# Performance work log

Hardware: AMD Instinct MI355X
Metric: run time of the kernel (lower is better)

## Reference

```python
import jax, jax.numpy as jnp
import numpy as np

B, F_IN, T = 128, 64, 512       # batch, input_features, seq_len
H, L = 512, 3                   # hidden_dim, num_layers
F_OUT, W_OUT = 8, 64            # output_features, output_window


def setup_inputs() -> dict:
    key = jax.random.key(0)
    ks = jax.random.split(key, 13)
    s = 1.0 / np.sqrt(H)  # torch nn.LSTM init scale
    f32 = jnp.float32
    return {
        "x": jax.random.normal(ks[0], (B, F_IN, T), f32),
        # encoder LSTM params (gate order i,f,g,o like torch)
        "enc_Wih0": jax.random.normal(ks[1], (4 * H, F_IN), f32) * s,
        "enc_Wih": jax.random.normal(ks[2], (L - 1, 4 * H, H), f32) * s,
        "enc_Whh": jax.random.normal(ks[3], (L, 4 * H, H), f32) * s,
        "enc_bih": jax.random.normal(ks[4], (L, 4 * H), f32) * s,
        "enc_bhh": jax.random.normal(ks[5], (L, 4 * H), f32) * s,
        # decoder LSTM params
        "dec_Wih0": jax.random.normal(ks[6], (4 * H, F_OUT), f32) * s,
        "dec_Wih": jax.random.normal(ks[7], (L - 1, 4 * H, H), f32) * s,
        "dec_Whh": jax.random.normal(ks[8], (L, 4 * H, H), f32) * s,
        "dec_bih": jax.random.normal(ks[9], (L, 4 * H), f32) * s,
        "dec_bhh": jax.random.normal(ks[10], (L, 4 * H), f32) * s,
        # output projection
        "fc_w": jax.random.normal(ks[11], (F_OUT, H), f32) * s,
        "fc_b": jax.random.normal(ks[12], (F_OUT,), f32) * s,
    }


def _cell(inp, h, c, Wi, Wh, bi, bh):
    # torch LSTM cell: gates = W_ih x + b_ih + W_hh h + b_hh, order i,f,g,o
    g = inp @ Wi.T + h @ Wh.T + bi + bh
    i, f, gg, o = jnp.split(g, 4, axis=-1)
    c_new = jax.nn.sigmoid(f) * c + jax.nn.sigmoid(i) * jnp.tanh(gg)
    h_new = jax.nn.sigmoid(o) * jnp.tanh(c_new)
    return h_new, c_new


def _stack_step(x_t, h, c, Wih0, Wih, Whh, bih, bhh):
    # one time step through all L layers; h,c: [L,B,H]
    inp = x_t
    hs, cs = [], []
    for l in range(Whh.shape[0]):
        Wi = Wih0 if l == 0 else Wih[l - 1]
        h_new, c_new = _cell(inp, h[l], c[l], Wi, Whh[l], bih[l], bhh[l])
        hs.append(h_new)
        cs.append(c_new)
        inp = h_new
    return jnp.stack(hs), jnp.stack(cs), inp


def reference(x, enc_Wih0, enc_Wih, enc_Whh, enc_bih, enc_bhh,
              dec_Wih0, dec_Wih, dec_Whh, dec_bih, dec_bhh, fc_w, fc_b):
    b = x.shape[0]
    # ---- encoder: x.permute(0,2,1) -> [B,T,F_IN], scan over time ----
    x_seq = jnp.transpose(x, (2, 0, 1))  # [T,B,F_IN]
    h0 = jnp.zeros((L, b, H), x.dtype)
    c0 = jnp.zeros((L, b, H), x.dtype)

    def enc_step(carry, x_t):
        h, c = carry
        h, c, _ = _stack_step(x_t, h, c, enc_Wih0, enc_Wih, enc_Whh, enc_bih, enc_bhh)
        return (h, c), None

    (h, c), _ = jax.lax.scan(enc_step, (h0, c0), x_seq)

    # ---- last_x = x[:, -1, :][:, 0:F_OUT] (target_coin_index=0) ----
    dec_in = x[:, -1, :F_OUT]  # [B, F_OUT]

    def dec_step(carry, _):
        h, c, inp = carry
        h, c, top = _stack_step(inp, h, c, dec_Wih0, dec_Wih, dec_Whh, dec_bih, dec_bhh)
        pred = top @ fc_w.T + fc_b  # [B, F_OUT]
        return (h, c, pred), pred

    _, preds = jax.lax.scan(dec_step, (h, c, dec_in), None, length=W_OUT)  # [W,B,F_OUT]
    # torch returns cat over time [B,W,F_OUT] then permute(0,2,1) -> [B,F_OUT,W]
    return jnp.transpose(preds, (1, 2, 0))
```

## Files before the change

kernel.cpp:

```cpp
#include <hip/hip_runtime.h>
#include <hip/hip_cooperative_groups.h>

namespace cg = cooperative_groups;

#define B_    128
#define H_    512
#define T_    512
#define FIN_  64
#define FOUT_ 8
#define WOUT_ 64
#define G4H_  2048

#define NBLK  192
#define NTHR  512
#define RD    4

typedef __attribute__((ext_vector_type(8))) _Float16 half8;
typedef __attribute__((ext_vector_type(4))) float f32x4;
typedef unsigned short u16;
typedef unsigned int u32;

#define LOSCALE   4096.0f
#define LOINV     0.000244140625f

struct Params {
  const float *x, *eWih0, *eWih, *eWhh, *ebih, *ebhh;
  const float *dWih0, *dWih, *dWhh, *dbih, *dbhh, *fcw, *fcb;
  float *out; float *ws;
};

__device__ __forceinline__ float sigm(float x) { return 1.0f / (1.0f + __expf(-x)); }
__device__ __forceinline__ float tanhf_(float x) {
  float e = __expf(-2.0f * fabsf(x));
  return copysignf((1.0f - e) / (1.0f + e), x);
}
__device__ __forceinline__ u16 h2u(_Float16 h) {
  union { _Float16 f; u16 u; } v; v.f = h; return v.u;
}
__device__ __forceinline__ void split16(float w, u16& hi, u16& lo) {
  _Float16 h = (_Float16)w;
  _Float16 l = (_Float16)((w - (float)h) * LOSCALE);
  hi = h2u(h); lo = h2u(l);
}

__device__ __forceinline__ int aload(const int* p) {
  return __hip_atomic_load(p, __ATOMIC_RELAXED, __HIP_MEMORY_SCOPE_AGENT);
}
__device__ __forceinline__ void wait_all(const int* a, const int* b, const int* c) {
  if (threadIdx.x == 0) {
    while (a && aload(a) < 64) __builtin_amdgcn_s_sleep(1);
    while (b && aload(b) < 64) __builtin_amdgcn_s_sleep(1);
    while (c && aload(c) < 64) __builtin_amdgcn_s_sleep(1);
    __threadfence();
  }
  __syncthreads();
}
__device__ __forceinline__ void signal_f(int* f) {
  __syncthreads();
  if (threadIdx.x == 0) {
    __threadfence();
    __hip_atomic_fetch_add(f, 1, __ATOMIC_RELAXED, __HIP_MEMORY_SCOPE_AGENT);
  }
}

__device__ void stage_w(u16* WbHi, u16* WbLo, const float* Wi, int Kreal, int K0pad,
                        const float* Wh, int j0) {
  const int rowlen = K0pad + H_;
  for (int n = 0; n < 32; ++n) {
    const int gr = (n >> 3) * H_ + j0 + (n & 7);
    const float* s0 = Wi + (size_t)gr * Kreal;
    const float* s1 = Wh + (size_t)gr * H_;
    const int sw = (n & 7) << 3;
    for (int k = threadIdx.x; k < rowlen; k += NTHR) {
      float w = (k < K0pad) ? ((k < Kreal) ? s0[k] : 0.0f) : s1[k - K0pad];
      u16 hi, lo; split16(w, hi, lo);
      int kk = k ^ sw;
      WbHi[n * 1024 + kk] = hi;
      WbLo[n * 1024 + kk] = lo;
    }
  }
}

template <int NC0, bool DEC0, bool FC>
__device__ __forceinline__ void cell(
    const u16* __restrict__ WbHi, const u16* __restrict__ WbLo,
    float* __restrict__ gl, float* __restrict__ predl,
    const float* __restrict__ bias_s, const float* __restrict__ fcw_s,
    const u16* __restrict__ i0h, const u16* __restrict__ i0l, const int ld0,
    const float* __restrict__ pr_in,
    const u16* __restrict__ iHh, const u16* __restrict__ iHl,
    u16* __restrict__ ohh, u16* __restrict__ ohl, const int j0,
    float* __restrict__ creg, float* __restrict__ pr_out) {
  const int tid = threadIdx.x;
  const int lane = tid & 63, lr = lane & 15, lg = lane >> 4;
  const int m0 = (tid >> 6) << 4;
  const int mb = m0 + lr;
  const int sw = (lr & 7) << 3;

  f32x4 acc0 = {0.f, 0.f, 0.f, 0.f}, acc1 = {0.f, 0.f, 0.f, 0.f};
  f32x4 acc0L = {0.f, 0.f, 0.f, 0.f}, acc1L = {0.f, 0.f, 0.f, 0.f};

  const u16* bh0 = WbHi + lr * 1024;
  const u16* bl0 = WbLo + lr * 1024;
  const u16* bh1 = WbHi + (16 + lr) * 1024;
  const u16* bl1 = WbLo + (16 + lr) * 1024;

  constexpr int K0PAD = NC0 * 32;

#define MFMA6(AH, AL, BO)                                                        \
  {                                                                              \
    half8 w0h = *(const half8*)(bh0 + (BO));                                     \
    half8 w0l = *(const half8*)(bl0 + (BO));                                     \
    half8 w1h = *(const half8*)(bh1 + (BO));                                     \
    half8 w1l = *(const half8*)(bl1 + (BO));                                     \
    acc0  = __builtin_amdgcn_mfma_f32_16x16x32_f16(AH, w0h, acc0, 0, 0, 0);      \
    acc1  = __builtin_amdgcn_mfma_f32_16x16x32_f16(AH, w1h, acc1, 0, 0, 0);      \
    acc0L = __builtin_amdgcn_mfma_f32_16x16x32_f16(AL, w0h, acc0L, 0, 0, 0);     \
    acc1L = __builtin_amdgcn_mfma_f32_16x16x32_f16(AL, w1h, acc1L, 0, 0, 0);     \
    acc0L = __builtin_amdgcn_mfma_f32_16x16x32_f16(AH, w0l, acc0L, 0, 0, 0);     \
    acc1L = __builtin_amdgcn_mfma_f32_16x16x32_f16(AH, w1l, acc1L, 0, 0, 0);     \
  }

  if constexpr (DEC0) {
    half8 ah = {}, al = {};
    if (lg == 0) {
      const f32x4 v0 = *(const f32x4*)(pr_in + mb * 8);
      const f32x4 v1 = *(const f32x4*)(pr_in + mb * 8 + 4);
      float v[8] = {v0[0], v0[1], v0[2], v0[3], v1[0], v1[1], v1[2], v1[3]};
      #pragma unroll
      for (int j = 0; j < 8; ++j) {
        _Float16 h = (_Float16)v[j];
        ah[j] = h;
        al[j] = (_Float16)((v[j] - (float)h) * LOSCALE);
      }
    }
    MFMA6(ah, al, ((lg << 3) ^ sw));
  } else {
    const u16* a0h = i0h + (size_t)mb * ld0 + lg * 8;
    const u16* a0l = i0l + (size_t)mb * ld0 + lg * 8;
    #pragma unroll 4
    for (int kk = 0; kk < NC0; ++kk) {
      half8 ah = *(const half8*)(a0h + kk * 32);
      half8 al = *(const half8*)(a0l + kk * 32);
      MFMA6(ah, al, (((kk * 4 + lg) << 3) ^ sw));
    }
  }
  {
    const u16* aHh = iHh + (size_t)mb * H_ + lg * 8;
    const u16* aHl = iHl + (size_t)mb * H_ + lg * 8;
    #pragma unroll 4
    for (int kk = 0; kk < 16; ++kk) {
      half8 ah = *(const half8*)(aHh + kk * 32);
      half8 al = *(const half8*)(aHl + kk * 32);
      MFMA6(ah, al, (((K0PAD / 8 + kk * 4 + lg) << 3) ^ sw));
    }
  }
#undef MFMA6

  #pragma unroll
  for (int i = 0; i < 4; ++i) {
    acc0[i] = fmaf(acc0L[i], LOINV, acc0[i]);
    acc1[i] = fmaf(acc1L[i], LOINV, acc1[i]);
  }

  const int mch = (m0 >> 2) + lg;
  *(f32x4*)(gl + lr * 128 + ((mch ^ (lr & 7)) << 2)) = acc0;
  *(f32x4*)(gl + (16 + lr) * 128 + ((mch ^ (lr & 7)) << 2)) = acc1;
  __syncthreads();

  const int b = tid & 127, c0 = (tid >> 7) << 1;
  float hv[2];
  #pragma unroll
  for (int u = 0; u < 2; ++u) {
    const int cc = c0 + u;
    const int bs = b >> 2, bo = b & 3;
    float gi = gl[(cc) * 128 + ((bs ^ (cc & 7)) << 2) + bo] + bias_s[cc];
    float gf = gl[(8 + cc) * 128 + ((bs ^ ((8 + cc) & 7)) << 2) + bo] + bias_s[8 + cc];
    float gg = gl[(16 + cc) * 128 + ((bs ^ ((16 + cc) & 7)) << 2) + bo] + bias_s[16 + cc];
    float go = gl[(24 + cc) * 128 + ((bs ^ ((24 + cc) & 7)) << 2) + bo] + bias_s[24 + cc];
    float cv = sigm(gf) * creg[u] + sigm(gi) * tanhf_(gg);
    creg[u] = cv;
    hv[u] = sigm(go) * tanhf_(cv);
  }
  u16 h0b, l0b, h1b, l1b;
  split16(hv[0], h0b, l0b);
  split16(hv[1], h1b, l1b);
  *(u32*)(ohh + (size_t)b * H_ + j0 + c0) = (u32)h0b | ((u32)h1b << 16);
  *(u32*)(ohl + (size_t)b * H_ + j0 + c0) = (u32)l0b | ((u32)l1b << 16);

  if constexpr (FC) {
    for (int i = tid; i < FOUT_ * B_; i += NTHR) predl[i] = 0.0f;
    __syncthreads();
    #pragma unroll
    for (int f = 0; f < 8; ++f)
      atomicAdd(&predl[b * 8 + f],
                hv[0] * fcw_s[f * 8 + c0] + hv[1] * fcw_s[f * 8 + c0 + 1]);
    __syncthreads();
    for (int i = tid; i < FOUT_ * B_; i += NTHR) atomicAdd(&pr_out[i], predl[i]);
  }
}

__global__ void __launch_bounds__(NTHR, 1) lstm_all(Params p) {
  __shared__ __align__(16) u16 WbHi[32 * 1024];
  __shared__ __align__(16) u16 WbLo[32 * 1024];
  __shared__ __align__(16) float gl[32 * B_];
  __shared__ float predl[FOUT_ * B_];
  __shared__ float bias_s[32];
  __shared__ float fcw_s[64];

  const int tid = threadIdx.x;
  const int bid = blockIdx.x;
  const int layer = bid >> 6;
  const int j0 = (bid & 63) * 8;
  const size_t HB = (size_t)B_ * H_;

  u16* xb = (u16*)p.ws;
  u16* ehb = xb + (size_t)2 * T_ * B_ * FIN_;
  u16* dhb = ehb + (size_t)3 * RD * 2 * HB;
  float* pr = (float*)(dhb + (size_t)3 * RD * 2 * HB);
  int* f_enc = (int*)(pr + (size_t)65 * B_ * FOUT_);
  int* f_dec = f_enc + 3 * 513;
  int* f_pred = f_dec + 3 * 65;

  cg::grid_group grid = cg::this_grid();
  const int gid = bid * NTHR + tid, gstep = NBLK * NTHR;

  for (int i = gid; i < 3 * 65536; i += gstep) {
    int l = i >> 16, off = i & 65535;
    ((u32*)ehb)[(size_t)l * (RD * 65536) + off] = 0u;
  }
  for (int i = gid; i < 3 * 513 + 3 * 65 + 65; i += gstep) f_enc[i] = 0;
  for (int i = gid; i < 65 * B_ * FOUT_; i += gstep) {
    int d = i >> 10, r = i & 1023, b = r >> 3, f = r & 7;
    pr[i] = (d == 0) ? p.x[((size_t)b * FIN_ + (FIN_ - 1)) * T_ + f] : p.fcb[f];
  }
  {
    const size_t XE0 = (size_t)T_ * B_ * FIN_;
    for (int i = gid; i < T_ * B_ * FIN_; i += gstep) {
      int t = i & 511, f = (i >> 9) & 63, b = i >> 15;
      float v = p.x[((size_t)b * FIN_ + f) * T_ + t];
      u16 hi, lo; split16(v, hi, lo);
      size_t o = ((size_t)t * B_ + b) * FIN_ + f;
      xb[o] = hi;
      xb[XE0 + o] = lo;
    }
  }
  if (layer == 0)      stage_w(WbHi, WbLo, p.eWih0, FIN_, FIN_, p.eWhh, j0);
  else if (layer == 1) stage_w(WbHi, WbLo, p.eWih, H_, H_, p.eWhh + (size_t)G4H_ * H_, j0);
  else                 stage_w(WbHi, WbLo, p.eWih + (size_t)G4H_ * H_, H_, H_,
                               p.eWhh + (size_t)2 * G4H_ * H_, j0);
  if (tid < 32) {
    int gr = (tid >> 3) * H_ + j0 + (tid & 7);
    bias_s[tid] = p.ebih[layer * G4H_ + gr] + p.ebhh[layer * G4H_ + gr];
  }
  grid.sync();

  float creg[2] = {0.0f, 0.0f};
  const size_t XE = (size_t)T_ * B_ * FIN_;
  auto ep = [&](int l, int idx, int pl) -> u16* {
    return ehb + (((size_t)l * RD + (idx & (RD - 1))) * 2 + pl) * HB;
  };
  auto dp = [&](int l, int idx, int pl) -> u16* {
    return dhb + (((size_t)l * RD + (idx & (RD - 1))) * 2 + pl) * HB;
  };

  for (int t = 0; t < T_; ++t) {
    const int* wsib = (t >= 1) ? &f_enc[layer * 513 + t] : nullptr;
    const int* wprod = (layer > 0) ? &f_enc[(layer - 1) * 513 + t + 1] : nullptr;
    const int* wbp = (layer < 2 && t >= RD) ? &f_enc[(layer + 1) * 513 + t - (RD - 1)]
                                            : nullptr;
    wait_all(wsib, wprod, wbp);
    if (layer == 0) {
      cell<2, false, false>(WbHi, WbLo, gl, predl, bias_s, fcw_s,
                            xb + (size_t)t * B_ * FIN_, xb + XE + (size_t)t * B_ * FIN_,
                            FIN_, nullptr,
                            ep(0, t, 0), ep(0, t, 1),
                            ep(0, t + 1, 0), ep(0, t + 1, 1), j0, creg, nullptr);
    } else {
      cell<16, false, false>(WbHi, WbLo, gl, predl, bias_s, fcw_s,
                             ep(layer - 1, t + 1, 0), ep(layer - 1, t + 1, 1), H_, nullptr,
                             ep(layer, t, 0), ep(layer, t, 1),
                             ep(layer, t + 1, 0), ep(layer, t + 1, 1), j0, creg, nullptr);
    }
    if (t == T_ - 1) {
      __syncthreads();
      const u32* src = (const u32*)ep(layer, T_, 0);
      u32* dst = (u32*)dp(layer, 0, 0);
      for (int i = tid; i < 1024; i += NTHR) {
        int pl = i >> 9, b = (i >> 2) & 127, w = i & 3;
        size_t o = (size_t)pl * (HB >> 1) + (size_t)b * (H_ >> 1) + (j0 >> 1) + w;
        dst[o] = src[o];
      }
      signal_f(&f_dec[layer * 65 + 0]);
    }
    signal_f(&f_enc[layer * 513 + t + 1]);
  }

  if (layer == 0)      stage_w(WbHi, WbLo, p.dWih0, FOUT_, 32, p.dWhh, j0);
  else if (layer == 1) stage_w(WbHi, WbLo, p.dWih, H_, H_, p.dWhh + (size_t)G4H_ * H_, j0);
  else                 stage_w(WbHi, WbLo, p.dWih + (size_t)G4H_ * H_, H_, H_,
                               p.dWhh + (size_t)2 * G4H_ * H_, j0);
  if (tid < 32) {
    int gr = (tid >> 3) * H_ + j0 + (tid & 7);
    bias_s[tid] = p.dbih[layer * G4H_ + gr] + p.dbhh[layer * G4H_ + gr];
  }
  if (layer == 2 && tid < 64)
    fcw_s[tid] = p.fcw[(size_t)(tid >> 3) * H_ + j0 + (tid & 7)];

  for (int d = 0; d < WOUT_; ++d) {
    if (layer == 0) {
      wait_all((d > 0) ? &f_pred[d] : nullptr,
               &f_dec[0 * 65 + d],
               (d >= RD) ? &f_dec[1 * 65 + d - (RD - 1)] : nullptr);
      cell<1, true, false>(WbHi, WbLo, gl, predl, bias_s, fcw_s,
                           nullptr, nullptr, 0, pr + (size_t)d * B_ * FOUT_,
                           dp(0, d, 0), dp(0, d, 1),
                           dp(0, d + 1, 0), dp(0, d + 1, 1), j0, creg, nullptr);
      signal_f(&f_dec[0 * 65 + d + 1]);
    } else if (layer == 1) {
      wait_all(&f_dec[1 * 65 + d], &f_dec[0 * 65 + d + 1],
               (d >= RD) ? &f_dec[2 * 65 + d - (RD - 1)] : nullptr);
      cell<16, false, false>(WbHi, WbLo, gl, predl, bias_s, fcw_s,
                             dp(0, d + 1, 0), dp(0, d + 1, 1), H_, nullptr,
                             dp(1, d, 0), dp(1, d, 1),
                             dp(1, d + 1, 0), dp(1, d + 1, 1), j0, creg, nullptr);
      signal_f(&f_dec[1 * 65 + d + 1]);
    } else {
      wait_all(&f_dec[2 * 65 + d], &f_dec[1 * 65 + d + 1], nullptr);
      cell<16, false, true>(WbHi, WbLo, gl, predl, bias_s, fcw_s,
                            dp(1, d + 1, 0), dp(1, d + 1, 1), H_, nullptr,
                            dp(2, d, 0), dp(2, d, 1),
                            dp(2, d + 1, 0), dp(2, d + 1, 1), j0, creg,
                            pr + (size_t)(d + 1) * B_ * FOUT_);
      __syncthreads();
      if (tid == 0) {
        __threadfence();
        __hip_atomic_fetch_add(&f_dec[2 * 65 + d + 1], 1, __ATOMIC_RELAXED,
                               __HIP_MEMORY_SCOPE_AGENT);
        __hip_atomic_fetch_add(&f_pred[d + 1], 1, __ATOMIC_RELAXED,
                               __HIP_MEMORY_SCOPE_AGENT);
      }
    }
  }

  if (layer == 0) {
    const int k = bid;
    if (k == WOUT_ - 1) wait_all(&f_pred[WOUT_], nullptr, nullptr);
    const float* s = pr + (size_t)(k + 1) * B_ * FOUT_;
    for (int i = tid; i < B_ * FOUT_; i += NTHR) {
      int b = i >> 3, f = i & 7;
      p.out[((size_t)b * FOUT_ + f) * WOUT_ + k] = s[i];
    }
  }
}

extern "C" void kernel_launch(void* const* d_in, const int* in_sizes, int n_in,
                              void* d_out, int out_size, void* d_ws, size_t ws_size,
                              hipStream_t stream) {
  (void)in_sizes; (void)n_in; (void)out_size; (void)ws_size;
  Params p;
  p.x     = (const float*)d_in[0];
  p.eWih0 = (const float*)d_in[1];
  p.eWih  = (const float*)d_in[2];
  p.eWhh  = (const float*)d_in[3];
  p.ebih  = (const float*)d_in[4];
  p.ebhh  = (const float*)d_in[5];
  p.dWih0 = (const float*)d_in[6];
  p.dWih  = (const float*)d_in[7];
  p.dWhh  = (const float*)d_in[8];
  p.dbih  = (const float*)d_in[9];
  p.dbhh  = (const float*)d_in[10];
  p.fcw   = (const float*)d_in[11];
  p.fcb   = (const float*)d_in[12];
  p.out   = (float*)d_out;
  p.ws    = (float*)d_ws;
  void* args[] = { &p };
  hipLaunchCooperativeKernel((const void*)lstm_all, dim3(NBLK), dim3(NTHR), args, 0,
                             stream);
}
```

Before: 21.91 ms.

## Replace atomic counter flags with per-block progress slots and retile MFMA loop

Synchronisation changes from shared fetch-add counters polled by one thread to per-block progress slots written with atomic stores. Each wave polls 64 slots in parallel, one slot per lane. The MFMA inner loop is also retiled so each wave reuses one weight fragment across two batch row tiles, with a 16-way LDS swizzle in place of the 8-way one. The goal is to reduce atomic contention and serial polling latency on the critical recurrent path, and to halve LDS weight reads. In exchange, each wait now issues more global loads, and the new flag semantics must keep producer and consumer ordering correct.

```diff
diff --git a/kernel.cpp b/kernel.cpp
--- a/kernel.cpp
+++ b/kernel.cpp
@@ -46,20 +46,21 @@
 __device__ __forceinline__ int aload(const int* p) {
   return __hip_atomic_load(p, __ATOMIC_RELAXED, __HIP_MEMORY_SCOPE_AGENT);
 }
-__device__ __forceinline__ void wait_all(const int* a, const int* b, const int* c) {
-  if (threadIdx.x == 0) {
-    while (a && aload(a) < 64) __builtin_amdgcn_s_sleep(1);
-    while (b && aload(b) < 64) __builtin_amdgcn_s_sleep(1);
-    while (c && aload(c) < 64) __builtin_amdgcn_s_sleep(1);
-    __threadfence();
-  }
+__device__ __forceinline__ void wait3(const int* a, int ta, const int* b, int tb,
+                                      const int* c, int tc) {
+  const int wv = threadIdx.x >> 6, s = threadIdx.x & 63;
+  if (wv == 0 && a)      { while (aload(a + s) < ta) __builtin_amdgcn_s_sleep(2); }
+  else if (wv == 1 && b) { while (aload(b + s) < tb) __builtin_amdgcn_s_sleep(2); }
+  else if (wv == 2 && c) { while (aload(c + s) < tc) __builtin_amdgcn_s_sleep(2); }
   __syncthreads();
-}
-__device__ __forceinline__ void signal_f(int* f) {
+  if (threadIdx.x == 0) __threadfence();
+  __syncthreads();
+}
+__device__ __forceinline__ void signal1(int* slot, int v) {
   __syncthreads();
   if (threadIdx.x == 0) {
     __threadfence();
-    __hip_atomic_fetch_add(f, 1, __ATOMIC_RELAXED, __HIP_MEMORY_SCOPE_AGENT);
+    __hip_atomic_store(slot, v, __ATOMIC_RELAXED, __HIP_MEMORY_SCOPE_AGENT);
   }
 }
 
@@ -70,11 +71,11 @@
     const int gr = (n >> 3) * H_ + j0 + (n & 7);
     const float* s0 = Wi + (size_t)gr * Kreal;
     const float* s1 = Wh + (size_t)gr * H_;
-    const int sw = (n & 7) << 3;
+    const int swz = n & 15;
     for (int k = threadIdx.x; k < rowlen; k += NTHR) {
       float w = (k < K0pad) ? ((k < Kreal) ? s0[k] : 0.0f) : s1[k - K0pad];
       u16 hi, lo; split16(w, hi, lo);
-      int kk = k ^ sw;
+      int kk = (k & 7) | ((((k >> 3) ^ swz)) << 3);
       WbHi[n * 1024 + kk] = hi;
       WbLo[n * 1024 + kk] = lo;
     }
@@ -93,79 +94,78 @@
     float* __restrict__ creg, float* __restrict__ pr_out) {
   const int tid = threadIdx.x;
   const int lane = tid & 63, lr = lane & 15, lg = lane >> 4;
-  const int m0 = (tid >> 6) << 4;
-  const int mb = m0 + lr;
-  const int sw = (lr & 7) << 3;
-
-  f32x4 acc0 = {0.f, 0.f, 0.f, 0.f}, acc1 = {0.f, 0.f, 0.f, 0.f};
-  f32x4 acc0L = {0.f, 0.f, 0.f, 0.f}, acc1L = {0.f, 0.f, 0.f, 0.f};
-
-  const u16* bh0 = WbHi + lr * 1024;
-  const u16* bl0 = WbLo + lr * 1024;
-  const u16* bh1 = WbHi + (16 + lr) * 1024;
-  const u16* bl1 = WbLo + (16 + lr) * 1024;
-
+  const int wv = tid >> 6, nt = wv >> 2, mq = wv & 3;
+  const int mb0 = mq * 32 + lr;
+  const int sw = lr;
+
+  f32x4 accA = {0.f,0.f,0.f,0.f}, accB = {0.f,0.f,0.f,0.f};
+  f32x4 accAL = {0.f,0.f,0.f,0.f}, accBL = {0.f,0.f,0.f,0.f};
+
+  const u16* bh = WbHi + (nt * 16 + lr) * 1024;
+  const u16* bl = WbLo + (nt * 16 + lr) * 1024;
   constexpr int K0PAD = NC0 * 32;
 
-#define MFMA6(AH, AL, BO)                                                        \
+#define MFMA6(AH0, AL0, AH1, AL1, CH)                                            \
   {                                                                              \
-    half8 w0h = *(const half8*)(bh0 + (BO));                                     \
-    half8 w0l = *(const half8*)(bl0 + (BO));                                     \
-    half8 w1h = *(const half8*)(bh1 + (BO));                                     \
-    half8 w1l = *(const half8*)(bl1 + (BO));                                     \
-    acc0  = __builtin_amdgcn_mfma_f32_16x16x32_f16(AH, w0h, acc0, 0, 0, 0);      \
-    acc1  = __builtin_amdgcn_mfma_f32_16x16x32_f16(AH, w1h, acc1, 0, 0, 0);      \
-    acc0L = __builtin_amdgcn_mfma_f32_16x16x32_f16(AL, w0h, acc0L, 0, 0, 0);     \
-    acc1L = __builtin_amdgcn_mfma_f32_16x16x32_f16(AL, w1h, acc1L, 0, 0, 0);     \
-    acc0L = __builtin_amdgcn_mfma_f32_16x16x32_f16(AH, w0l, acc0L, 0, 0, 0);     \
-    acc1L = __builtin_amdgcn_mfma_f32_16x16x32_f16(AH, w1l, acc1L, 0, 0, 0);     \
+    half8 wh = *(const half8*)(bh + (((CH) ^ sw) << 3));                         \
+    half8 wl = *(const half8*)(bl + (((CH) ^ sw) << 3));                         \
+    accA  = __builtin_amdgcn_mfma_f32_16x16x32_f16(AH0, wh, accA, 0, 0, 0);      \
+    accB  = __builtin_amdgcn_mfma_f32_16x16x32_f16(AH1, wh, accB, 0, 0, 0);      \
+    accAL = __builtin_amdgcn_mfma_f32_16x16x32_f16(AL0, wh, accAL, 0, 0, 0);     \
+    accBL = __builtin_amdgcn_mfma_f32_16x16x32_f16(AL1, wh, accBL, 0, 0, 0);     \
+    accAL = __builtin_amdgcn_mfma_f32_16x16x32_f16(AH0, wl, accAL, 0, 0, 0);     \
+    accBL = __builtin_amdgcn_mfma_f32_16x16x32_f16(AH1, wl, accBL, 0, 0, 0);     \
   }
 
   if constexpr (DEC0) {
-    half8 ah = {}, al = {};
+    half8 ah0 = {}, al0 = {}, ah1 = {}, al1 = {};
     if (lg == 0) {
-      const f32x4 v0 = *(const f32x4*)(pr_in + mb * 8);
-      const f32x4 v1 = *(const f32x4*)(pr_in + mb * 8 + 4);
-      float v[8] = {v0[0], v0[1], v0[2], v0[3], v1[0], v1[1], v1[2], v1[3]};
       #pragma unroll
       for (int j = 0; j < 8; ++j) {
-        _Float16 h = (_Float16)v[j];
-        ah[j] = h;
-        al[j] = (_Float16)((v[j] - (float)h) * LOSCALE);
+        float v0 = pr_in[mb0 * 8 + j], v1 = pr_in[(mb0 + 16) * 8 + j];
+        _Float16 h0 = (_Float16)v0, h1 = (_Float16)v1;
+        ah0[j] = h0; al0[j] = (_Float16)((v0 - (float)h0) * LOSCALE);
+        ah1[j] = h1; al1[j] = (_Float16)((v1 - (float)h1) * LOSCALE);
       }
     }
-    MFMA6(ah, al, ((lg << 3) ^ sw));
+    MFMA6(ah0, al0, ah1, al1, lg);
   } else {
-    const u16* a0h = i0h + (size_t)mb * ld0 + lg * 8;
-    const u16* a0l = i0l + (size_t)mb * ld0 + lg * 8;
-    #pragma unroll 4
+    const u16* a0h = i0h + (size_t)mb0 * ld0 + lg * 8;
+    const u16* a0l = i0l + (size_t)mb0 * ld0 + lg * 8;
+    const int st = 16 * ld0;
+    #pragma unroll
     for (int kk = 0; kk < NC0; ++kk) {
-      half8 ah = *(const half8*)(a0h + kk * 32);
-      half8 al = *(const half8*)(a0l + kk * 32);
-      MFMA6(ah, al, (((kk * 4 + lg) << 3) ^ sw));
+      half8 ah0 = *(const half8*)(a0h + kk * 32);
+      half8 al0 = *(const half8*)(a0l + kk * 32);
+      half8 ah1 = *(const half8*)(a0h + st + kk * 32);
+      half8 al1 = *(const half8*)(a0l + st + kk * 32);
+      MFMA6(ah0, al0, ah1, al1, kk * 4 + lg);
     }
   }
   {
-    const u16* aHh = iHh + (size_t)mb * H_ + lg * 8;
-    const u16* aHl = iHl + (size_t)mb * H_ + lg * 8;
-    #pragma unroll 4
+    const u16* aHh = iHh + (size_t)mb0 * H_ + lg * 8;
+    const u16* aHl = iHl + (size_t)mb0 * H_ + lg * 8;
+    const int st = 16 * H_;
+    #pragma unroll
     for (int kk = 0; kk < 16; ++kk) {
-      half8 ah = *(const half8*)(aHh + kk * 32);
-      half8 al = *(const half8*)(aHl + kk * 32);
-      MFMA6(ah, al, (((K0PAD / 8 + kk * 4 + lg) << 3) ^ sw));
+      half8 ah0 = *(const half8*)(aHh + kk * 32);
+      half8 al0 = *(const half8*)(aHl + kk * 32);
+      half8 ah1 = *(const half8*)(aHh + st + kk * 32);
+      half8 al1 = *(const half8*)(aHl + st + kk * 32);
+      MFMA6(ah0, al0, ah1, al1, K0PAD / 8 + kk * 4 + lg);
     }
   }
 #undef MFMA6
 
   #pragma unroll
   for (int i = 0; i < 4; ++i) {
-    acc0[i] = fmaf(acc0L[i], LOINV, acc0[i]);
-    acc1[i] = fmaf(acc1L[i], LOINV, acc1[i]);
-  }
-
-  const int mch = (m0 >> 2) + lg;
-  *(f32x4*)(gl + lr * 128 + ((mch ^ (lr & 7)) << 2)) = acc0;
-  *(f32x4*)(gl + (16 + lr) * 128 + ((mch ^ (lr & 7)) << 2)) = acc1;
+    accA[i] = fmaf(accAL[i], LOINV, accA[i]);
+    accB[i] = fmaf(accBL[i], LOINV, accB[i]);
+  }
+
+  const int row = nt * 16 + lr, rsw = row & 7;
+  *(f32x4*)(gl + row * 128 + (((mq * 8 + lg) ^ rsw) << 2)) = accA;
+  *(f32x4*)(gl + row * 128 + (((mq * 8 + 4 + lg) ^ rsw) << 2)) = accB;
   __syncthreads();
 
   const int b = tid & 127, c0 = (tid >> 7) << 1;
@@ -211,7 +211,8 @@
   const int tid = threadIdx.x;
   const int bid = blockIdx.x;
   const int layer = bid >> 6;
-  const int j0 = (bid & 63) * 8;
+  const int blk = bid & 63;
+  const int j0 = blk * 8;
   const size_t HB = (size_t)B_ * H_;
 
   u16* xb = (u16*)p.ws;
@@ -219,8 +220,7 @@
   u16* dhb = ehb + (size_t)3 * RD * 2 * HB;
   float* pr = (float*)(dhb + (size_t)3 * RD * 2 * HB);
   int* f_enc = (int*)(pr + (size_t)65 * B_ * FOUT_);
-  int* f_dec = f_enc + 3 * 513;
-  int* f_pred = f_dec + 3 * 65;
+  int* f_dec = f_enc + 3 * 64;
 
   cg::grid_group grid = cg::this_grid();
   const int gid = bid * NTHR + tid, gstep = NBLK * NTHR;
@@ -229,7 +229,7 @@
     int l = i >> 16, off = i & 65535;
     ((u32*)ehb)[(size_t)l * (RD * 65536) + off] = 0u;
   }
-  for (int i = gid; i < 3 * 513 + 3 * 65 + 65; i += gstep) f_enc[i] = 0;
+  for (int i = gid; i < 3 * 64; i += gstep) { f_enc[i] = 0; f_dec[i] = -1; }
   for (int i = gid; i < 65 * B_ * FOUT_; i += gstep) {
     int d = i >> 10, r = i & 1023, b = r >> 3, f = r & 7;
     pr[i] = (d == 0) ? p.x[((size_t)b * FIN_ + (FIN_ - 1)) * T_ + f] : p.fcb[f];
@@ -265,11 +265,9 @@
   };
 
   for (int t = 0; t < T_; ++t) {
-    const int* wsib = (t >= 1) ? &f_enc[layer * 513 + t] : nullptr;
-    const int* wprod = (layer > 0) ? &f_enc[(layer - 1) * 513 + t + 1] : nullptr;
-    const int* wbp = (layer < 2 && t >= RD) ? &f_enc[(layer + 1) * 513 + t - (RD - 1)]
-                                            : nullptr;
-    wait_all(wsib, wprod, wbp);
+    wait3(f_enc + layer * 64, t,
+          (layer > 0) ? f_enc + (layer - 1) * 64 : nullptr, t + 1,
+          (layer < 2 && t >= RD) ? f_enc + (layer + 1) * 64 : nullptr, t - (RD - 1));
     if (layer == 0) {
       cell<2, false, false>(WbHi, WbLo, gl, predl, bias_s, fcw_s,
                             xb + (size_t)t * B_ * FIN_, xb + XE + (size_t)t * B_ * FIN_,
@@ -291,9 +289,17 @@
         size_t o = (size_t)pl * (HB >> 1) + (size_t)b * (H_ >> 1) + (j0 >> 1) + w;
         dst[o] = src[o];
       }
-      signal_f(&f_dec[layer * 65 + 0]);
-    }
-    signal_f(&f_enc[layer * 513 + t + 1]);
+      __syncthreads();
+      if (tid == 0) {
+        __threadfence();
+        __hip_atomic_store(&f_dec[layer * 64 + blk], 0, __ATOMIC_RELAXED,
+                           __HIP_MEMORY_SCOPE_AGENT);
+        __hip_atomic_store(&f_enc[layer * 64 + blk], T_, __ATOMIC_RELAXED,
+                           __HIP_MEMORY_SCOPE_AGENT);
+      }
+    } else {
+      signal1(&f_enc[layer * 64 + blk], t + 1);
+    }
   }
 
   if (layer == 0)      stage_w(WbHi, WbLo, p.dWih0, FOUT_, 32, p.dWhh, j0);
@@ -309,43 +315,37 @@
 
   for (int d = 0; d < WOUT_; ++d) {
     if (layer == 0) {
-      wait_all((d > 0) ? &f_pred[d] : nullptr,
-               &f_dec[0 * 65 + d],
-               (d >= RD) ? &f_dec[1 * 65 + d - (RD - 1)] : nullptr);
+      wait3(f_dec + 0 * 64, d,
+            (d > 0) ? f_dec + 2 * 64 : nullptr, d,
+            (d >= RD) ? f_dec + 1 * 64 : nullptr, d - (RD - 1));
       cell<1, true, false>(WbHi, WbLo, gl, predl, bias_s, fcw_s,
                            nullptr, nullptr, 0, pr + (size_t)d * B_ * FOUT_,
                            dp(0, d, 0), dp(0, d, 1),
                            dp(0, d + 1, 0), dp(0, d + 1, 1), j0, creg, nullptr);
-      signal_f(&f_dec[0 * 65 + d + 1]);
+      signal1(&f_dec[0 * 64 + blk], d + 1);
     } else if (layer == 1) {
-      wait_all(&f_dec[1 * 65 + d], &f_dec[0 * 65 + d + 1],
-               (d >= RD) ? &f_dec[2 * 65 + d - (RD - 1)] : nullptr);
+      wait3(f_dec + 1 * 64, d,
+            f_dec + 0 * 64, d + 1,
+            (d >= RD) ? f_dec + 2 * 64 : nullptr, d - (RD - 1));
       cell<16, false, false>(WbHi, WbLo, gl, predl, bias_s, fcw_s,
                              dp(0, d + 1, 0), dp(0, d + 1, 1), H_, nullptr,
                              dp(1, d, 0), dp(1, d, 1),
                              dp(1, d + 1, 0), dp(1, d + 1, 1), j0, creg, nullptr);
-      signal_f(&f_dec[1 * 65 + d + 1]);
+      signal1(&f_dec[1 * 64 + blk], d + 1);
     } else {
-      wait_all(&f_dec[2 * 65 + d], &f_dec[1 * 65 + d + 1], nullptr);
+      wait3(f_dec + 2 * 64, d, f_dec + 1 * 64, d + 1, nullptr, 0);
       cell<16, false, true>(WbHi, WbLo, gl, predl, bias_s, fcw_s,
                             dp(1, d + 1, 0), dp(1, d + 1, 1), H_, nullptr,
                             dp(2, d, 0), dp(2, d, 1),
                             dp(2, d + 1, 0), dp(2, d + 1, 1), j0, creg,
                             pr + (size_t)(d + 1) * B_ * FOUT_);
-      __syncthreads();
-      if (tid == 0) {
-        __threadfence();
-        __hip_atomic_fetch_add(&f_dec[2 * 65 + d + 1], 1, __ATOMIC_RELAXED,
-                               __HIP_MEMORY_SCOPE_AGENT);
-        __hip_atomic_fetch_add(&f_pred[d + 1], 1, __ATOMIC_RELAXED,
-                               __HIP_MEMORY_SCOPE_AGENT);
-      }
+      signal1(&f_dec[2 * 64 + blk], d + 1);
     }
   }
 
   if (layer == 0) {
     const int k = bid;
-    if (k == WOUT_ - 1) wait_all(&f_pred[WOUT_], nullptr, nullptr);
+    if (k == WOUT_ - 1) wait3(f_dec + 2 * 64, WOUT_, nullptr, 0, nullptr, 0);
     const float* s = pr + (size_t)(k + 1) * B_ * FOUT_;
     for (int i = tid; i < B_ * FOUT_; i += NTHR) {
       int b = i >> 3, f = i & 7;
```

Result: slower. 27.54 ms (+25.7%).
